# Performance work log

Measured on AMD Instinct MI355X. Metric: run time of the kernel, lower is better.

## Reference

```python
import jax, jax.numpy as jnp
import numpy as np

T_BINS = 1000  # max_time_bins
N_HEADS = 8
BIN = 64


def _ln(x, g, b):
    m = x.mean(-1, keepdims=True)
    v = ((x - m) ** 2).mean(-1, keepdims=True)
    return (x - m) / jnp.sqrt(v + 1e-5) * g + b


def _time_attn(h, td, mask, wq, bq, wk, bk, wv, bv, wo, bo, temb):
    # h: [B,S,D], td: [B,S] float, mask: [B,S] bool
    B, S, D = h.shape
    dk = D // N_HEADS
    q = (h @ wq + bq).reshape(B, S, N_HEADS, dk)
    k = (h @ wk + bk).reshape(B, S, N_HEADS, dk)
    v = (h @ wv + bv).reshape(B, S, N_HEADS, dk)
    scores = jnp.einsum('bqhd,bkhd->bhqk', q, k) / jnp.sqrt(jnp.float32(dk))
    tb = jnp.clip(td.astype(jnp.int32), 0, T_BINS - 1)
    bias = temb[tb].transpose(0, 2, 1)[:, :, None, :]  # [B,H,1,S], key-position bias
    scores = jnp.where(mask[:, None, None, :], scores + bias, -1e9)
    attn = jax.nn.softmax(scores, axis=-1)
    ctx = jnp.einsum('bhqk,bkhd->bqhd', attn, v).reshape(B, S, D)
    return ctx @ wo + bo


def _forward(x, time_deltas,
             emb_event, emb_rel, emb_abs,
             iq_w, iq_b, ik_w, ik_b, iv_w, iv_b, io_w, io_b, i_temb, i_g, i_bt,
             eq_w, eq_b, ek_w, ek_b, ev_w, ev_b, eo_w, eo_b, e_temb, e_g, e_bt,
             w1, b1, w2, b2):
    B, S = x.shape
    NB = S // BIN  # S chosen as a multiple of bin_size -> no padding
    mask = x != 0  # padding_idx = 0
    ee = emb_event.at[0].set(0.0)  # padding_idx row is zero
    rel_bins = jnp.clip(time_deltas.astype(jnp.int32), 0, T_BINS - 1)
    abs_t = jnp.cumsum(jnp.clip(time_deltas, 0.0, None), axis=1)
    abs_bins = jnp.clip(abs_t.astype(jnp.int32), 0, T_BINS - 1)
    h = ee[x] + emb_rel[rel_bins] + emb_abs[abs_bins]  # [B,S,D]
    D = h.shape[-1]
    # intra-bin attention over [B*NB, BIN]
    hi = h.reshape(B * NB, BIN, D)
    ti = time_deltas.reshape(B * NB, BIN)
    mi = mask.reshape(B * NB, BIN)
    hi = _ln(_time_attn(hi, ti, mi, iq_w, iq_b, ik_w, ik_b, iv_w, iv_b, io_w, io_b, i_temb), i_g, i_bt)
    hi = hi.reshape(B, NB, BIN, D)
    # mean pool per bin over valid tokens
    mb = mask.reshape(B, NB, BIN)
    w = mb[..., None].astype(h.dtype)
    denom = jnp.maximum(w.sum(2), 1.0)
    bin_repr = (hi * w).sum(2) / denom  # [B,NB,D]
    bin_mask = mb.any(2)
    abs_masked = jnp.where(mb, abs_t.reshape(B, NB, BIN), 0.0)
    bin_abs = abs_masked.max(2)
    bin_rel = jnp.concatenate(
        [jnp.zeros((B, 1), h.dtype), jnp.maximum(bin_abs[:, 1:] - bin_abs[:, :-1], 0.0)], axis=1)
    h_inter = _ln(_time_attn(bin_repr, bin_rel, bin_mask,
                             eq_w, eq_b, ek_w, ek_b, ev_w, ev_b, eo_w, eo_b, e_temb), e_g, e_bt)
    last_idx = jnp.clip(bin_mask.sum(1) - 1, 0, None)
    last = h_inter[jnp.arange(B), last_idx]  # [B,D]
    return jax.nn.sigmoid(jax.nn.relu(last @ w1 + b1) @ w2 + b2)  # [B,1]


def setup_inputs() -> dict:
    key = jax.random.key(0)
    ks = jax.random.split(key, 24)
    B, S, D, V = 8, 4096, 512, 20000
    sc = 1.0 / np.sqrt(D)
    f32 = jnp.float32
    inp = {
        'x': jax.random.randint(ks[0], (B, S), 0, V),
        'time_deltas': jax.random.uniform(ks[1], (B, S), f32) * 10.0,
        'emb_event': jax.random.normal(ks[2], (V, D), f32) * 0.02,
        'emb_rel': jax.random.normal(ks[3], (T_BINS, D), f32) * 0.02,
        'emb_abs': jax.random.normal(ks[4], (T_BINS, D), f32) * 0.02,
    }
    names = ['iq', 'ik', 'iv', 'io', 'eq', 'ek', 'ev', 'eo']
    for i, n in enumerate(names):
        inp[n + '_w'] = jax.random.normal(ks[5 + i], (D, D), f32) * sc
        inp[n + '_b'] = jnp.zeros((D,), f32)
    inp['i_temb'] = jax.random.normal(ks[13], (T_BINS, N_HEADS), f32) * 0.02
    inp['e_temb'] = jax.random.normal(ks[14], (T_BINS, N_HEADS), f32) * 0.02
    inp['i_g'] = jnp.ones((D,), f32); inp['i_bt'] = jnp.zeros((D,), f32)
    inp['e_g'] = jnp.ones((D,), f32); inp['e_bt'] = jnp.zeros((D,), f32)
    inp['w1'] = jax.random.normal(ks[15], (D, D // 2), f32) * sc
    inp['b1'] = jnp.zeros((D // 2,), f32)
    inp['w2'] = jax.random.normal(ks[16], (D // 2, 1), f32) * np.sqrt(2.0 / D)
    inp['b2'] = jnp.zeros((1,), f32)
    return inp


def reference(x, time_deltas, emb_event, emb_rel, emb_abs,
              iq_w, iq_b, ik_w, ik_b, iv_w, iv_b, io_w, io_b, i_temb, i_g, i_bt,
              eq_w, eq_b, ek_w, ek_b, ev_w, ev_b, eo_w, eo_b, e_temb, e_g, e_bt,
              w1, b1, w2, b2):
    return _forward(x, time_deltas, emb_event, emb_rel, emb_abs,
                    iq_w, iq_b, ik_w, ik_b, iv_w, iv_b, io_w, io_b, i_temb, i_g, i_bt,
                    eq_w, eq_b, ek_w, ek_b, ev_w, ev_b, eo_w, eo_b, e_temb, e_g, e_bt,
                    w1, b1, w2, b2)
```

## Files before the change

kernel.cpp:

```cpp
#include <hip/hip_runtime.h>


typedef __attribute__((ext_vector_type(8))) short bf16x8;
typedef __attribute__((ext_vector_type(4))) float f32x4;

#define DEVI __device__ __forceinline__

DEVI unsigned short f2bf(float f) {
  union { float f; unsigned u; } v; v.f = f;
  unsigned r = v.u + 0x7FFFu + ((v.u >> 16) & 1u);
  return (unsigned short)(r >> 16);
}
DEVI float bf2f(unsigned short u) {
  union { unsigned u; float f; } v; v.u = ((unsigned)u) << 16; return v.f;
}

#define GLOAD_LDS16(gp, lp) \
  __builtin_amdgcn_global_load_lds((const __attribute__((address_space(1))) void*)(gp), \
                                   (__attribute__((address_space(3))) void*)(lp), 16, 0, 0)

struct TPackArgs { const float* s[8]; unsigned short* d[8];
                   const float* bs[6]; float* bd[2]; };

__global__ __launch_bounds__(256) void k_tpack8(TPackArgs args) {
  __shared__ float tile[64][65];
  if (blockIdx.x == 512) {
    int t = threadIdx.x;
    for (int i = t; i < 1536; i += 256) {
      int sel = i >> 9, r = i & 511;
      args.bd[0][i] = args.bs[sel][r];
      args.bd[1][i] = args.bs[3 + sel][r];
    }
    return;
  }
  int mat = blockIdx.x >> 6;
  int tl = blockIdx.x & 63;
  const float* W = args.s[mat];
  unsigned short* Wt = args.d[mat];
  int n0 = (tl & 7) << 6, k0 = (tl >> 3) << 6;
  int t = threadIdx.x, j = t & 63, i0 = t >> 6;
#pragma unroll
  for (int rr = 0; rr < 16; ++rr) {
    int i = rr * 4 + i0;
    tile[i][j] = W[(size_t)(k0 + i) * 512 + n0 + j];
  }
  __syncthreads();
#pragma unroll
  for (int rr = 0; rr < 16; ++rr) {
    int i = rr * 4 + i0;
    Wt[(size_t)(n0 + i) * 512 + k0 + j] = f2bf(tile[j][i]);
  }
}

__global__ __launch_bounds__(64) void k_time(const float* __restrict__ td, const int* __restrict__ x,
    float* __restrict__ abs_t, float* __restrict__ bin_rel, int* __restrict__ bin_mask,
    int* __restrict__ last_idx) {
  int b = blockIdx.x, lane = threadIdx.x;
  const float* row = td + (size_t)b * 4096 + lane * 64;
  const int*   xr  = x  + (size_t)b * 4096 + lane * 64;
  float* out = abs_t + (size_t)b * 4096 + lane * 64;
  float s = 0.f;
  for (int i = 0; i < 64; ++i) s += fmaxf(row[i], 0.f);
  float pre = s;
#pragma unroll
  for (int off = 1; off < 64; off <<= 1) {
    float n = __shfl_up(pre, off, 64);
    if (lane >= off) pre += n;
  }
  float a = pre - s;
  float am = 0.f; int anyv = 0;
  for (int i = 0; i < 64; ++i) {
    a += fmaxf(row[i], 0.f);
    out[i] = a;
    if (xr[i] != 0) { am = fmaxf(am, a); anyv = 1; }
  }
  float prev = __shfl_up(am, 1, 64);
  bin_rel[b * 64 + lane] = (lane == 0) ? 0.f : fmaxf(am - prev, 0.f);
  bin_mask[b * 64 + lane] = anyv;
  unsigned long long bal = __ballot(anyv != 0);
  if (lane == 0) last_idx[b] = max(__popcll(bal) - 1, 0);
}

__global__ __launch_bounds__(256) void k_embed(const int* __restrict__ x, const float* __restrict__ td,
    const float* __restrict__ abs_t, const float* __restrict__ ee, const float* __restrict__ er,
    const float* __restrict__ ea, unsigned short* __restrict__ h) {
  int t = threadIdx.x;
  int tok = blockIdx.x * 4 + (t >> 6);
  int lane = t & 63;
  int c0 = lane * 8;
  int xi = x[tok];
  int rb = (int)td[tok]; rb = min(max(rb, 0), 999);
  int ab = (int)abs_t[tok]; ab = min(max(ab, 0), 999);
  const f32x4* pr = (const f32x4*)(er + (size_t)rb * 512 + c0);
  const f32x4* pa = (const f32x4*)(ea + (size_t)ab * 512 + c0);
  f32x4 s0 = pr[0] + pa[0];
  f32x4 s1 = pr[1] + pa[1];
  if (xi != 0) {
    const f32x4* pe = (const f32x4*)(ee + (size_t)xi * 512 + c0);
    s0 += pe[0]; s1 += pe[1];
  }
  bf16x8 o;
#pragma unroll
  for (int i = 0; i < 4; ++i) { o[i] = (short)f2bf(s0[i]); o[4 + i] = (short)f2bf(s1[i]); }
  *(bf16x8*)(h + (size_t)tok * 512 + c0) = o;
}

DEVI bf16x8 lds_frag32(const unsigned short* buf, int r, int g) {
  int sr = r >> 1;
  int slot = (((r & 1) << 2) | g) ^ (sr & 7);
  return *(const bf16x8*)&buf[sr * 64 + slot * 8];
}

__global__ __launch_bounds__(512, 2) void k_gemm256(const unsigned short* __restrict__ A,
    const unsigned short* __restrict__ Wt, const float* __restrict__ bias,
    unsigned short* __restrict__ Cout, int N, int tiles_n) {
  __shared__ unsigned short lds[4][2][256 * 32];
  int bid = blockIdx.x;
  { int q = (int)gridDim.x >> 3; bid = (bid & 7) * q + (bid >> 3); }
  int by = bid / tiles_n, bx = bid % tiles_n;
  int m0 = by << 8, n0 = bx << 8;
  int t = threadIdx.x;
  int lane = t & 63, w = t >> 6;
  int wm = w >> 2, wn = w & 3;
  int l15 = lane & 15, l4 = lane >> 4;

  auto stageA = [&](int kt) {
    int k0 = kt << 5;
    unsigned short* dst = &lds[kt & 3][0][0];
#pragma unroll
    for (int l = 0; l < 2; ++l) {
      int pos = l * 512 + t;
      int sr = pos >> 3, slot = pos & 7;
      int gp = slot ^ (sr & 7);
      int row = sr * 2 + (gp >> 2);
      GLOAD_LDS16(&A[(size_t)(m0 + row) * 512 + k0 + (gp & 3) * 8], dst + pos * 8);
    }
  };
  auto stageB = [&](int kt) {
    int k0 = kt << 5;
    unsigned short* dst = &lds[kt & 3][1][0];
#pragma unroll
    for (int l = 0; l < 2; ++l) {
      int pos = l * 512 + t;
      int sr = pos >> 3, slot = pos & 7;
      int gp = slot ^ (sr & 7);
      int row = sr * 2 + (gp >> 2);
      GLOAD_LDS16(&Wt[(size_t)(n0 + row) * 512 + k0 + (gp & 3) * 8], dst + pos * 8);
    }
  };

  f32x4 acc[8][4] = {};
  stageA(0); stageB(0);
  stageA(1); stageB(1);
  stageA(2); stageB(2);

  for (int kt = 0; kt < 16; ++kt) {
    if (kt < 14)       asm volatile("s_waitcnt vmcnt(8)" ::: "memory");
    else if (kt == 14) asm volatile("s_waitcnt vmcnt(4)" ::: "memory");
    else               asm volatile("s_waitcnt vmcnt(0)" ::: "memory");
    __builtin_amdgcn_s_barrier();
    const unsigned short* As = &lds[kt & 3][0][0];
    const unsigned short* Bs = &lds[kt & 3][1][0];

    bf16x8 af[4], bb[4];
#pragma unroll
    for (int i = 0; i < 4; ++i) af[i] = lds_frag32(As, wm * 128 + i * 16 + l15, l4);
#pragma unroll
    for (int j = 0; j < 4; ++j) bb[j] = lds_frag32(Bs, wn * 64 + j * 16 + l15, l4);
    if (kt < 13) stageA(kt + 3);
    __builtin_amdgcn_sched_barrier(0);
    __builtin_amdgcn_s_barrier();
    asm volatile("s_waitcnt lgkmcnt(0)" ::: "memory");
    __builtin_amdgcn_sched_barrier(0);
    __builtin_amdgcn_s_setprio(1);
#pragma unroll
    for (int i = 0; i < 4; ++i)
#pragma unroll
      for (int j = 0; j < 4; ++j)
        acc[i][j] = __builtin_amdgcn_mfma_f32_16x16x32_bf16(af[i], bb[j], acc[i][j], 0, 0, 0);
    __builtin_amdgcn_s_setprio(0);

    bf16x8 ah[4];
#pragma unroll
    for (int i = 0; i < 4; ++i) ah[i] = lds_frag32(As, wm * 128 + 64 + i * 16 + l15, l4);
    if (kt < 13) stageB(kt + 3);
    __builtin_amdgcn_sched_barrier(0);
    __builtin_amdgcn_s_barrier();
    asm volatile("s_waitcnt lgkmcnt(0)" ::: "memory");
    __builtin_amdgcn_sched_barrier(0);
    __builtin_amdgcn_s_setprio(1);
#pragma unroll
    for (int i = 0; i < 4; ++i)
#pragma unroll
      for (int j = 0; j < 4; ++j)
        acc[4 + i][j] = __builtin_amdgcn_mfma_f32_16x16x32_bf16(ah[i], bb[j], acc[4 + i][j], 0, 0, 0);
    __builtin_amdgcn_s_setprio(0);
  }
#pragma unroll
  for (int i = 0; i < 8; ++i) {
    int rowb = m0 + wm * 128 + i * 16 + (l4 << 2);
#pragma unroll
    for (int j = 0; j < 4; ++j) {
      int col = n0 + wn * 64 + j * 16 + l15;
      float bv = bias[col];
#pragma unroll
      for (int r = 0; r < 4; ++r)
        Cout[(size_t)(rowb + r) * N + col] = f2bf(acc[i][j][r] + bv);
    }
  }
}

__global__ __launch_bounds__(256) void k_gemm(const unsigned short* __restrict__ A,
    const unsigned short* __restrict__ Wt, const float* __restrict__ bias,
    unsigned short* __restrict__ Cout, int N, int tiles_n) {
  __shared__ unsigned short As[128 * 72];
  __shared__ unsigned short Bs[128 * 72];
  int bx = blockIdx.x % tiles_n;
  int by = blockIdx.x / tiles_n;
  int m0 = by << 7, n0 = bx << 7;
  int t = threadIdx.x;
  int lane = t & 63, w = t >> 6;
  int wm = w >> 1, wn = w & 1;
  f32x4 acc[4][4] = {};
  for (int k0 = 0; k0 < 512; k0 += 64) {
    __syncthreads();
#pragma unroll
    for (int i = 0; i < 4; ++i) {
      int idx = t + i * 256;
      int row = idx >> 3, seg = idx & 7;
      *(bf16x8*)&As[row * 72 + seg * 8] = *(const bf16x8*)&A[(size_t)(m0 + row) * 512 + k0 + seg * 8];
      *(bf16x8*)&Bs[row * 72 + seg * 8] = *(const bf16x8*)&Wt[(size_t)(n0 + row) * 512 + k0 + seg * 8];
    }
    __syncthreads();
#pragma unroll
    for (int ks = 0; ks < 2; ++ks) {
      bf16x8 af[4], bb[4];
#pragma unroll
      for (int i = 0; i < 4; ++i) {
        af[i] = *(const bf16x8*)&As[(wm * 64 + i * 16 + (lane & 15)) * 72 + ks * 32 + (lane >> 4) * 8];
        bb[i] = *(const bf16x8*)&Bs[(wn * 64 + i * 16 + (lane & 15)) * 72 + ks * 32 + (lane >> 4) * 8];
      }
#pragma unroll
      for (int i = 0; i < 4; ++i)
#pragma unroll
        for (int j = 0; j < 4; ++j)
          acc[i][j] = __builtin_amdgcn_mfma_f32_16x16x32_bf16(af[i], bb[j], acc[i][j], 0, 0, 0);
    }
  }
#pragma unroll
  for (int i = 0; i < 4; ++i) {
    int rowb = m0 + wm * 64 + i * 16 + ((lane >> 4) << 2);
#pragma unroll
    for (int j = 0; j < 4; ++j) {
      int col = n0 + wn * 64 + j * 16 + (lane & 15);
      float bv = bias[col];
#pragma unroll
      for (int r = 0; r < 4; ++r)
        Cout[(size_t)(rowb + r) * N + col] = f2bf(acc[i][j][r] + bv);
    }
  }
}

__global__ __launch_bounds__(256) void k_attn(const unsigned short* __restrict__ qkv,
    const float* __restrict__ td, const int* __restrict__ validv,
    const float* __restrict__ temb, unsigned short* __restrict__ ctx) {
  __shared__ float bias_s[4][64];
  __shared__ int valid_s[64];
  __shared__ unsigned short P_s[4][64][72];
  __shared__ unsigned short Vt_s[4][64][72];
  int blk = blockIdx.x >> 1, hg = blockIdx.x & 1;
  int t = threadIdx.x, hl = t >> 6, lane = t & 63;
  int h = hg * 4 + hl;
  size_t base = (size_t)blk * 64;
  if (t < 64) {
    valid_s[t] = (validv[base + t] != 0) ? 1 : 0;
    int tb = (int)td[base + t];
    tb = min(max(tb, 0), 999);
#pragma unroll
    for (int hh = 0; hh < 4; ++hh) bias_s[hh][t] = temb[tb * 8 + hg * 4 + hh];
  }
  {
    const unsigned short* vp = qkv + (base + lane) * 1536 + 1024 + h * 64;
#pragma unroll
    for (int f8 = 0; f8 < 8; ++f8) {
      bf16x8 v8 = *(const bf16x8*)(vp + f8 * 8);
#pragma unroll
      for (int j = 0; j < 8; ++j) Vt_s[hl][f8 * 8 + j][lane] = (unsigned short)v8[j];
    }
  }
  __syncthreads();
  bf16x8 qa[2][4], kb[2][4];
#pragma unroll
  for (int ks = 0; ks < 2; ++ks)
#pragma unroll
    for (int i = 0; i < 4; ++i) {
      int row = i * 16 + (lane & 15);
      int kk = ks * 32 + (lane >> 4) * 8;
      qa[ks][i] = *(const bf16x8*)&qkv[(base + row) * 1536 + h * 64 + kk];
      kb[ks][i] = *(const bf16x8*)&qkv[(base + row) * 1536 + 512 + h * 64 + kk];
    }
  f32x4 acc[4][4] = {};
#pragma unroll
  for (int ks = 0; ks < 2; ++ks)
#pragma unroll
    for (int i = 0; i < 4; ++i)
#pragma unroll
      for (int j = 0; j < 4; ++j)
        acc[i][j] = __builtin_amdgcn_mfma_f32_16x16x32_bf16(qa[ks][i], kb[ks][j], acc[i][j], 0, 0, 0);
#pragma unroll
  for (int i = 0; i < 4; ++i) {
#pragma unroll
    for (int r = 0; r < 4; ++r) {
      float sv[4];
#pragma unroll
      for (int j = 0; j < 4; ++j) {
        int key = j * 16 + (lane & 15);
        float s = acc[i][j][r] * 0.125f;
        sv[j] = valid_s[key] ? (s + bias_s[hl][key]) : -1e9f;
      }
      float m = fmaxf(fmaxf(sv[0], sv[1]), fmaxf(sv[2], sv[3]));
#pragma unroll
      for (int off = 1; off < 16; off <<= 1) m = fmaxf(m, __shfl_xor(m, off, 64));
      float p[4], sum = 0.f;
#pragma unroll
      for (int j = 0; j < 4; ++j) { p[j] = __expf(sv[j] - m); sum += p[j]; }
#pragma unroll
      for (int off = 1; off < 16; off <<= 1) sum += __shfl_xor(sum, off, 64);
      float inv = 1.f / sum;
      int row = i * 16 + ((lane >> 4) << 2) + r;
#pragma unroll
      for (int j = 0; j < 4; ++j) P_s[hl][row][j * 16 + (lane & 15)] = f2bf(p[j] * inv);
    }
  }
  __syncthreads();
  f32x4 acc2[4][4] = {};
#pragma unroll
  for (int ks = 0; ks < 2; ++ks) {
    bf16x8 pa[4], vb[4];
    int kk = ks * 32 + (lane >> 4) * 8;
#pragma unroll
    for (int i = 0; i < 4; ++i) {
      pa[i] = *(const bf16x8*)&P_s[hl][i * 16 + (lane & 15)][kk];
      vb[i] = *(const bf16x8*)&Vt_s[hl][i * 16 + (lane & 15)][kk];
    }
#pragma unroll
    for (int i = 0; i < 4; ++i)
#pragma unroll
      for (int j = 0; j < 4; ++j)
        acc2[i][j] = __builtin_amdgcn_mfma_f32_16x16x32_bf16(pa[i], vb[j], acc2[i][j], 0, 0, 0);
  }
#pragma unroll
  for (int i = 0; i < 4; ++i) {
    int rowb = i * 16 + ((lane >> 4) << 2);
#pragma unroll
    for (int j = 0; j < 4; ++j) {
      int col = h * 64 + j * 16 + (lane & 15);
#pragma unroll
      for (int r = 0; r < 4; ++r)
        ctx[(base + rowb + r) * 512 + col] = f2bf(acc2[i][j][r]);
    }
  }
}

__global__ __launch_bounds__(256) void k_lnpool(const unsigned short* __restrict__ X,
    const float* __restrict__ g, const float* __restrict__ bt,
    const int* __restrict__ validv, unsigned short* __restrict__ out) {
  __shared__ float pool_s[4][512];
  __shared__ int cnt_s[4];
  int blk = blockIdx.x;
  int t = threadIdx.x, w = t >> 6, lane = t & 63;
  float gv[8], bv[8];
#pragma unroll
  for (int i = 0; i < 8; ++i) { gv[i] = g[lane * 8 + i]; bv[i] = bt[lane * 8 + i]; }
  float psum[8] = {0.f, 0.f, 0.f, 0.f, 0.f, 0.f, 0.f, 0.f};
  int cnt = 0;
  for (int r0 = 0; r0 < 16; ++r0) {
    int row = blk * 64 + w * 16 + r0;
    bf16x8 xv = *(const bf16x8*)(X + (size_t)row * 512 + lane * 8);
    float xa[8];
#pragma unroll
    for (int i = 0; i < 8; ++i) xa[i] = bf2f((unsigned short)xv[i]);
    float s = 0.f;
#pragma unroll
    for (int i = 0; i < 8; ++i) s += xa[i];
#pragma unroll
    for (int off = 1; off < 64; off <<= 1) s += __shfl_xor(s, off, 64);
    float mean = s * (1.f / 512.f);
    float vsum = 0.f;
#pragma unroll
    for (int i = 0; i < 8; ++i) { float d = xa[i] - mean; vsum += d * d; }
#pragma unroll
    for (int off = 1; off < 64; off <<= 1) vsum += __shfl_xor(vsum, off, 64);
    float rstd = rsqrtf(vsum * (1.f / 512.f) + 1e-5f);
    if (validv[row] != 0) {
      cnt++;
#pragma unroll
      for (int i = 0; i < 8; ++i) psum[i] += (xa[i] - mean) * rstd * gv[i] + bv[i];
    }
  }
#pragma unroll
  for (int i = 0; i < 8; ++i) pool_s[w][lane * 8 + i] = psum[i];
  if (lane == 0) cnt_s[w] = cnt;
  __syncthreads();
  int total = cnt_s[0] + cnt_s[1] + cnt_s[2] + cnt_s[3];
  float denom = fmaxf((float)total, 1.f);
  for (int c = t; c < 512; c += 256) {
    float v = (pool_s[0][c] + pool_s[1][c] + pool_s[2][c] + pool_s[3][c]) / denom;
    out[(size_t)blk * 512 + c] = f2bf(v);
  }
}

__global__ __launch_bounds__(256) void k_final(const unsigned short* __restrict__ proj2,
    const int* __restrict__ last_idx, const float* __restrict__ g, const float* __restrict__ bt,
    const float* __restrict__ w1, const float* __restrict__ b1,
    const float* __restrict__ w2, const float* __restrict__ b2, float* __restrict__ outp) {
  __shared__ float row_s[512];
  __shared__ float red_s[4];
  __shared__ float red2_s[4];
  int b = blockIdx.x, t = threadIdx.x;
  const unsigned short* rp = proj2 + (size_t)(b * 64 + last_idx[b]) * 512;
  float v0 = bf2f(rp[t]), v1 = bf2f(rp[t + 256]);
  float s = v0 + v1;
#pragma unroll
  for (int off = 1; off < 64; off <<= 1) s += __shfl_xor(s, off, 64);
  if ((t & 63) == 0) red_s[t >> 6] = s;
  __syncthreads();
  float mean = (red_s[0] + red_s[1] + red_s[2] + red_s[3]) * (1.f / 512.f);
  float d0 = v0 - mean, d1 = v1 - mean;
  float vs = d0 * d0 + d1 * d1;
#pragma unroll
  for (int off = 1; off < 64; off <<= 1) vs += __shfl_xor(vs, off, 64);
  if ((t & 63) == 0) red2_s[t >> 6] = vs;
  __syncthreads();
  float rstd = rsqrtf((red2_s[0] + red2_s[1] + red2_s[2] + red2_s[3]) * (1.f / 512.f) + 1e-5f);
  row_s[t]       = d0 * rstd * g[t]       + bt[t];
  row_s[t + 256] = d1 * rstd * g[t + 256] + bt[t + 256];
  __syncthreads();
  float acc = b1[t];
  for (int k = 0; k < 512; ++k) acc += row_s[k] * w1[(size_t)k * 256 + t];
  float hv = fmaxf(acc, 0.f) * w2[t];
#pragma unroll
  for (int off = 1; off < 64; off <<= 1) hv += __shfl_xor(hv, off, 64);
  if ((t & 63) == 0) red_s[t >> 6] = hv;
  __syncthreads();
  if (t == 0) {
    float o = red_s[0] + red_s[1] + red_s[2] + red_s[3] + b2[0];
    outp[b] = 1.f / (1.f + __expf(-o));
  }
}

extern "C" void kernel_launch(void* const* d_in, const int* in_sizes, int n_in,
                              void* d_out, int out_size, void* d_ws, size_t ws_size,
                              hipStream_t stream) {
  const int*   x    = (const int*)d_in[0];
  const float* td   = (const float*)d_in[1];
  const float* ee   = (const float*)d_in[2];
  const float* er   = (const float*)d_in[3];
  const float* ea   = (const float*)d_in[4];
  const float* iq_w = (const float*)d_in[5];  const float* iq_b = (const float*)d_in[6];
  const float* ik_w = (const float*)d_in[7];  const float* ik_b = (const float*)d_in[8];
  const float* iv_w = (const float*)d_in[9];  const float* iv_b = (const float*)d_in[10];
  const float* io_w = (const float*)d_in[11]; const float* io_b = (const float*)d_in[12];
  const float* eq_w = (const float*)d_in[13]; const float* eq_b = (const float*)d_in[14];
  const float* ek_w = (const float*)d_in[15]; const float* ek_b = (const float*)d_in[16];
  const float* ev_w = (const float*)d_in[17]; const float* ev_b = (const float*)d_in[18];
  const float* eo_w = (const float*)d_in[19]; const float* eo_b = (const float*)d_in[20];
  const float* i_temb = (const float*)d_in[21];
  const float* e_temb = (const float*)d_in[22];
  const float* i_g  = (const float*)d_in[23]; const float* i_bt = (const float*)d_in[24];
  const float* e_g  = (const float*)d_in[25]; const float* e_bt = (const float*)d_in[26];
  const float* w1   = (const float*)d_in[27]; const float* b1   = (const float*)d_in[28];
  const float* w2   = (const float*)d_in[29]; const float* b2   = (const float*)d_in[30];

  char* ws = (char*)d_ws;
  size_t off = 0;
  auto alloc = [&](size_t nb) { size_t r = off; off += (nb + 255) & ~(size_t)255; return r; };
  float* abs_t    = (float*)(ws + alloc((size_t)32768 * 4));
  float* bin_rel  = (float*)(ws + alloc(512 * 4));
  int*   bin_mask = (int*)(ws + alloc(512 * 4));
  int*   last_idx = (int*)(ws + alloc(64));
  unsigned short* wqkv_i = (unsigned short*)(ws + alloc((size_t)1536 * 512 * 2));
  unsigned short* wo_i   = (unsigned short*)(ws + alloc((size_t)512 * 512 * 2));
  unsigned short* wqkv_e = (unsigned short*)(ws + alloc((size_t)1536 * 512 * 2));
  unsigned short* wo_e   = (unsigned short*)(ws + alloc((size_t)512 * 512 * 2));
  float* bqkv_i = (float*)(ws + alloc(1536 * 4));
  float* bqkv_e = (float*)(ws + alloc(1536 * 4));
  unsigned short* hbuf = (unsigned short*)(ws + alloc((size_t)32768 * 512 * 2));
  char* big = ws + alloc((size_t)32768 * 1536 * 2);
  unsigned short* qkvbuf = (unsigned short*)big;
  unsigned short* projbuf = (unsigned short*)big;
  unsigned short* bin_repr = (unsigned short*)(ws + alloc((size_t)512 * 512 * 2));
  char* small = ws + alloc((size_t)512 * 1536 * 2);
  unsigned short* qkv2 = (unsigned short*)small;
  unsigned short* proj2 = (unsigned short*)small;
  unsigned short* ctx2 = (unsigned short*)(ws + alloc((size_t)512 * 512 * 2));

  TPackArgs tp;
  tp.s[0] = iq_w; tp.d[0] = wqkv_i;
  tp.s[1] = ik_w; tp.d[1] = wqkv_i + (size_t)512 * 512;
  tp.s[2] = iv_w; tp.d[2] = wqkv_i + (size_t)1024 * 512;
  tp.s[3] = io_w; tp.d[3] = wo_i;
  tp.s[4] = eq_w; tp.d[4] = wqkv_e;
  tp.s[5] = ek_w; tp.d[5] = wqkv_e + (size_t)512 * 512;
  tp.s[6] = ev_w; tp.d[6] = wqkv_e + (size_t)1024 * 512;
  tp.s[7] = eo_w; tp.d[7] = wo_e;
  tp.bs[0] = iq_b; tp.bs[1] = ik_b; tp.bs[2] = iv_b;
  tp.bs[3] = eq_b; tp.bs[4] = ek_b; tp.bs[5] = ev_b;
  tp.bd[0] = bqkv_i; tp.bd[1] = bqkv_e;
  k_tpack8<<<513, 256, 0, stream>>>(tp);

  k_time<<<8, 64, 0, stream>>>(td, x, abs_t, bin_rel, bin_mask, last_idx);

  k_embed<<<8192, 256, 0, stream>>>(x, td, abs_t, ee, er, ea, hbuf);

  k_gemm256<<<128 * 6, 512, 0, stream>>>(hbuf, wqkv_i, bqkv_i, qkvbuf, 1536, 6);
  k_attn<<<1024, 256, 0, stream>>>(qkvbuf, td, x, i_temb, hbuf);
  k_gemm256<<<128 * 2, 512, 0, stream>>>(hbuf, wo_i, io_b, projbuf, 512, 2);
  k_lnpool<<<512, 256, 0, stream>>>(projbuf, i_g, i_bt, x, bin_repr);

  k_gemm<<<4 * 12, 256, 0, stream>>>(bin_repr, wqkv_e, bqkv_e, qkv2, 1536, 12);
  k_attn<<<16, 256, 0, stream>>>(qkv2, bin_rel, bin_mask, e_temb, ctx2);
  k_gemm<<<4 * 4, 256, 0, stream>>>(ctx2, wo_e, eo_b, proj2, 512, 4);

  k_final<<<8, 256, 0, stream>>>(proj2, last_idx, e_g, e_bt, w1, b1, w2, b2, (float*)d_out);
}
```

Measured before the change: 234.2 us.

## Fuse intra-bin output projection with LayerNorm and mean pooling

Result: no change. 231.1 us (-1.3%).

```diff
diff --git a/kernel.cpp b/kernel.cpp
--- a/kernel.cpp
+++ b/kernel.cpp
@@ -85,24 +85,27 @@
     const float* __restrict__ abs_t, const float* __restrict__ ee, const float* __restrict__ er,
     const float* __restrict__ ea, unsigned short* __restrict__ h) {
   int t = threadIdx.x;
-  int tok = blockIdx.x * 4 + (t >> 6);
   int lane = t & 63;
   int c0 = lane * 8;
-  int xi = x[tok];
-  int rb = (int)td[tok]; rb = min(max(rb, 0), 999);
-  int ab = (int)abs_t[tok]; ab = min(max(ab, 0), 999);
-  const f32x4* pr = (const f32x4*)(er + (size_t)rb * 512 + c0);
-  const f32x4* pa = (const f32x4*)(ea + (size_t)ab * 512 + c0);
-  f32x4 s0 = pr[0] + pa[0];
-  f32x4 s1 = pr[1] + pa[1];
-  if (xi != 0) {
-    const f32x4* pe = (const f32x4*)(ee + (size_t)xi * 512 + c0);
-    s0 += pe[0]; s1 += pe[1];
-  }
-  bf16x8 o;
-#pragma unroll
-  for (int i = 0; i < 4; ++i) { o[i] = (short)f2bf(s0[i]); o[4 + i] = (short)f2bf(s1[i]); }
-  *(bf16x8*)(h + (size_t)tok * 512 + c0) = o;
+#pragma unroll
+  for (int it = 0; it < 4; ++it) {
+    int tok = blockIdx.x * 16 + it * 4 + (t >> 6);
+    int xi = x[tok];
+    int rb = (int)td[tok]; rb = min(max(rb, 0), 999);
+    int ab = (int)abs_t[tok]; ab = min(max(ab, 0), 999);
+    const f32x4* pr = (const f32x4*)(er + (size_t)rb * 512 + c0);
+    const f32x4* pa = (const f32x4*)(ea + (size_t)ab * 512 + c0);
+    f32x4 s0 = pr[0] + pa[0];
+    f32x4 s1 = pr[1] + pa[1];
+    if (xi != 0) {
+      const f32x4* pe = (const f32x4*)(ee + (size_t)xi * 512 + c0);
+      s0 += pe[0]; s1 += pe[1];
+    }
+    bf16x8 o;
+#pragma unroll
+    for (int i = 0; i < 4; ++i) { o[i] = (short)f2bf(s0[i]); o[4 + i] = (short)f2bf(s1[i]); }
+    *(bf16x8*)(h + (size_t)tok * 512 + c0) = o;
+  }
 }
 
 DEVI bf16x8 lds_frag32(const unsigned short* buf, int r, int g) {
@@ -168,7 +171,6 @@
 #pragma unroll
     for (int j = 0; j < 4; ++j) bb[j] = lds_frag32(Bs, wn * 64 + j * 16 + l15, l4);
     if (kt < 13) stageA(kt + 3);
-    __builtin_amdgcn_sched_barrier(0);
     __builtin_amdgcn_s_barrier();
     asm volatile("s_waitcnt lgkmcnt(0)" ::: "memory");
     __builtin_amdgcn_sched_barrier(0);
@@ -184,7 +186,6 @@
 #pragma unroll
     for (int i = 0; i < 4; ++i) ah[i] = lds_frag32(As, wm * 128 + 64 + i * 16 + l15, l4);
     if (kt < 13) stageB(kt + 3);
-    __builtin_amdgcn_sched_barrier(0);
     __builtin_amdgcn_s_barrier();
     asm volatile("s_waitcnt lgkmcnt(0)" ::: "memory");
     __builtin_amdgcn_sched_barrier(0);
@@ -206,6 +207,174 @@
 #pragma unroll
       for (int r = 0; r < 4; ++r)
         Cout[(size_t)(rowb + r) * N + col] = f2bf(acc[i][j][r] + bv);
+    }
+  }
+}
+
+__global__ __launch_bounds__(512, 2) void k_oproj(const unsigned short* __restrict__ ctx,
+    const unsigned short* __restrict__ WoT, const float* __restrict__ bo,
+    const int* __restrict__ x, const float* __restrict__ g, const float* __restrict__ bt,
+    unsigned short* __restrict__ bin_repr) {
+  __shared__ unsigned short ldsA[4][128 * 32];
+  __shared__ unsigned short ldsB[2][512 * 32];
+  int bid = blockIdx.x;
+  { int q = (int)gridDim.x >> 3; bid = (bid & 7) * q + (bid >> 3); }
+  int m0 = bid << 7;
+  int t = threadIdx.x;
+  int lane = t & 63, w = t >> 6;
+  int l15 = lane & 15, l4 = lane >> 4;
+
+  auto stageA = [&](int kt) {
+    int k0 = kt << 5;
+    unsigned short* dst = &ldsA[kt & 3][0];
+    int pos = t;
+    int sr = pos >> 3, slot = pos & 7;
+    int gp = slot ^ (sr & 7);
+    int row = sr * 2 + (gp >> 2);
+    GLOAD_LDS16(&ctx[(size_t)(m0 + row) * 512 + k0 + (gp & 3) * 8], dst + pos * 8);
+  };
+  auto stageB = [&](int kt) {
+    int k0 = kt << 5;
+    unsigned short* dst = &ldsB[kt & 1][0];
+#pragma unroll
+    for (int l = 0; l < 4; ++l) {
+      int pos = l * 512 + t;
+      int sr = pos >> 3, slot = pos & 7;
+      int gp = slot ^ (sr & 7);
+      int row = sr * 2 + (gp >> 2);
+      GLOAD_LDS16(&WoT[(size_t)row * 512 + k0 + (gp & 3) * 8], dst + pos * 8);
+    }
+  };
+
+  f32x4 acc[8][4] = {};
+  stageB(0); stageA(0); stageA(1); stageA(2); stageB(1);
+
+  for (int kt = 0; kt < 16; ++kt) {
+    if (kt == 0)      asm volatile("s_waitcnt vmcnt(6)" ::: "memory");
+    else if (kt < 14) asm volatile("s_waitcnt vmcnt(1)" ::: "memory");
+    else              asm volatile("s_waitcnt vmcnt(0)" ::: "memory");
+    __builtin_amdgcn_s_barrier();
+    const unsigned short* As = &ldsA[kt & 3][0];
+    const unsigned short* Bs = &ldsB[kt & 1][0];
+
+    bf16x8 af[4], bb[4];
+#pragma unroll
+    for (int i = 0; i < 4; ++i) af[i] = lds_frag32(As, i * 16 + l15, l4);
+#pragma unroll
+    for (int j = 0; j < 4; ++j) bb[j] = lds_frag32(Bs, w * 64 + j * 16 + l15, l4);
+    if (kt >= 1 && kt <= 14) stageB(kt + 1);
+    __builtin_amdgcn_s_barrier();
+    asm volatile("s_waitcnt lgkmcnt(0)" ::: "memory");
+    __builtin_amdgcn_sched_barrier(0);
+    __builtin_amdgcn_s_setprio(1);
+#pragma unroll
+    for (int i = 0; i < 4; ++i)
+#pragma unroll
+      for (int j = 0; j < 4; ++j)
+        acc[i][j] = __builtin_amdgcn_mfma_f32_16x16x32_bf16(af[i], bb[j], acc[i][j], 0, 0, 0);
+    __builtin_amdgcn_s_setprio(0);
+
+    bf16x8 ah[4];
+#pragma unroll
+    for (int i = 0; i < 4; ++i) ah[i] = lds_frag32(As, 64 + i * 16 + l15, l4);
+    if (kt <= 12) stageA(kt + 3);
+    __builtin_amdgcn_s_barrier();
+    asm volatile("s_waitcnt lgkmcnt(0)" ::: "memory");
+    __builtin_amdgcn_sched_barrier(0);
+    __builtin_amdgcn_s_setprio(1);
+#pragma unroll
+    for (int i = 0; i < 4; ++i)
+#pragma unroll
+      for (int j = 0; j < 4; ++j)
+        acc[4 + i][j] = __builtin_amdgcn_mfma_f32_16x16x32_bf16(ah[i], bb[j], acc[4 + i][j], 0, 0, 0);
+    __builtin_amdgcn_s_setprio(0);
+  }
+
+  __syncthreads();
+  float* red   = (float*)&ldsA[0][0];
+  float* meanL = red + 128 * 9;
+  float* rstdL = meanL + 128;
+  int*   valL  = (int*)(rstdL + 128);
+  int*   cntL  = valL + 128;
+
+  int cols[4]; float bov[4], gv[4], bv[4];
+#pragma unroll
+  for (int j = 0; j < 4; ++j) {
+    cols[j] = w * 64 + j * 16 + l15;
+    bov[j] = bo[cols[j]]; gv[j] = g[cols[j]]; bv[j] = bt[cols[j]];
+  }
+  if (t < 128) {
+    int v = (x[m0 + t] != 0) ? 1 : 0;
+    valL[t] = v;
+    unsigned long long bal = __ballot(v != 0);
+    if ((t & 63) == 0) cntL[t >> 6] = __popcll(bal);
+  }
+#pragma unroll
+  for (int i = 0; i < 8; ++i)
+#pragma unroll
+    for (int r = 0; r < 4; ++r) {
+      float s = (acc[i][0][r] + bov[0]) + (acc[i][1][r] + bov[1]) +
+                (acc[i][2][r] + bov[2]) + (acc[i][3][r] + bov[3]);
+#pragma unroll
+      for (int off = 1; off < 16; off <<= 1) s += __shfl_xor(s, off, 64);
+      if (l15 == 0) red[(i * 16 + l4 * 4 + r) * 9 + w] = s;
+    }
+  __syncthreads();
+  if (t < 128) {
+    float m = 0.f;
+#pragma unroll
+    for (int ww = 0; ww < 8; ++ww) m += red[t * 9 + ww];
+    meanL[t] = m * (1.f / 512.f);
+  }
+  __syncthreads();
+#pragma unroll
+  for (int i = 0; i < 8; ++i)
+#pragma unroll
+    for (int r = 0; r < 4; ++r) {
+      float m = meanL[i * 16 + l4 * 4 + r];
+      float s = 0.f;
+#pragma unroll
+      for (int j = 0; j < 4; ++j) { float d = acc[i][j][r] + bov[j] - m; s += d * d; }
+#pragma unroll
+      for (int off = 1; off < 16; off <<= 1) s += __shfl_xor(s, off, 64);
+      if (l15 == 0) red[(i * 16 + l4 * 4 + r) * 9 + w] = s;
+    }
+  __syncthreads();
+  if (t < 128) {
+    float vsum = 0.f;
+#pragma unroll
+    for (int ww = 0; ww < 8; ++ww) vsum += red[t * 9 + ww];
+    rstdL[t] = rsqrtf(vsum * (1.f / 512.f) + 1e-5f);
+  }
+  __syncthreads();
+  float p0[4] = {0.f, 0.f, 0.f, 0.f}, p1[4] = {0.f, 0.f, 0.f, 0.f};
+#pragma unroll
+  for (int i = 0; i < 8; ++i)
+#pragma unroll
+    for (int r = 0; r < 4; ++r) {
+      int row = i * 16 + l4 * 4 + r;
+      if (valL[row]) {
+        float m = meanL[row], rs = rstdL[row];
+#pragma unroll
+        for (int j = 0; j < 4; ++j) {
+          float y = (acc[i][j][r] + bov[j] - m) * rs * gv[j] + bv[j];
+          if (i < 4) p0[j] += y; else p1[j] += y;
+        }
+      }
+    }
+#pragma unroll
+  for (int j = 0; j < 4; ++j) {
+    p0[j] += __shfl_xor(p0[j], 16, 64); p0[j] += __shfl_xor(p0[j], 32, 64);
+    p1[j] += __shfl_xor(p1[j], 16, 64); p1[j] += __shfl_xor(p1[j], 32, 64);
+  }
+  float d0 = 1.f / fmaxf((float)cntL[0], 1.f);
+  float d1 = 1.f / fmaxf((float)cntL[1], 1.f);
+  if (l4 == 0) {
+    int binr = (m0 >> 6);
+#pragma unroll
+    for (int j = 0; j < 4; ++j) {
+      bin_repr[(size_t)binr * 512 + cols[j]]       = f2bf(p0[j] * d0);
+      bin_repr[(size_t)(binr + 1) * 512 + cols[j]] = f2bf(p1[j] * d1);
     }
   }
 }
@@ -359,54 +528,6 @@
       for (int r = 0; r < 4; ++r)
         ctx[(base + rowb + r) * 512 + col] = f2bf(acc2[i][j][r]);
     }
-  }
-}
-
-__global__ __launch_bounds__(256) void k_lnpool(const unsigned short* __restrict__ X,
-    const float* __restrict__ g, const float* __restrict__ bt,
-    const int* __restrict__ validv, unsigned short* __restrict__ out) {
-  __shared__ float pool_s[4][512];
-  __shared__ int cnt_s[4];
-  int blk = blockIdx.x;
-  int t = threadIdx.x, w = t >> 6, lane = t & 63;
-  float gv[8], bv[8];
-#pragma unroll
-  for (int i = 0; i < 8; ++i) { gv[i] = g[lane * 8 + i]; bv[i] = bt[lane * 8 + i]; }
-  float psum[8] = {0.f, 0.f, 0.f, 0.f, 0.f, 0.f, 0.f, 0.f};
-  int cnt = 0;
-  for (int r0 = 0; r0 < 16; ++r0) {
-    int row = blk * 64 + w * 16 + r0;
-    bf16x8 xv = *(const bf16x8*)(X + (size_t)row * 512 + lane * 8);
-    float xa[8];
-#pragma unroll
-    for (int i = 0; i < 8; ++i) xa[i] = bf2f((unsigned short)xv[i]);
-    float s = 0.f;
-#pragma unroll
-    for (int i = 0; i < 8; ++i) s += xa[i];
-#pragma unroll
-    for (int off = 1; off < 64; off <<= 1) s += __shfl_xor(s, off, 64);
-    float mean = s * (1.f / 512.f);
-    float vsum = 0.f;
-#pragma unroll
-    for (int i = 0; i < 8; ++i) { float d = xa[i] - mean; vsum += d * d; }
-#pragma unroll
-    for (int off = 1; off < 64; off <<= 1) vsum += __shfl_xor(vsum, off, 64);
-    float rstd = rsqrtf(vsum * (1.f / 512.f) + 1e-5f);
-    if (validv[row] != 0) {
-      cnt++;
-#pragma unroll
-      for (int i = 0; i < 8; ++i) psum[i] += (xa[i] - mean) * rstd * gv[i] + bv[i];
-    }
-  }
-#pragma unroll
-  for (int i = 0; i < 8; ++i) pool_s[w][lane * 8 + i] = psum[i];
-  if (lane == 0) cnt_s[w] = cnt;
-  __syncthreads();
-  int total = cnt_s[0] + cnt_s[1] + cnt_s[2] + cnt_s[3];
-  float denom = fmaxf((float)total, 1.f);
-  for (int c = t; c < 512; c += 256) {
-    float v = (pool_s[0][c] + pool_s[1][c] + pool_s[2][c] + pool_s[3][c]) / denom;
-    out[(size_t)blk * 512 + c] = f2bf(v);
   }
 }
 
@@ -486,9 +607,7 @@
   float* bqkv_i = (float*)(ws + alloc(1536 * 4));
   float* bqkv_e = (float*)(ws + alloc(1536 * 4));
   unsigned short* hbuf = (unsigned short*)(ws + alloc((size_t)32768 * 512 * 2));
-  char* big = ws + alloc((size_t)32768 * 1536 * 2);
-  unsigned short* qkvbuf = (unsigned short*)big;
-  unsigned short* projbuf = (unsigned short*)big;
+  unsigned short* qkvbuf = (unsigned short*)(ws + alloc((size_t)32768 * 1536 * 2));
   unsigned short* bin_repr = (unsigned short*)(ws + alloc((size_t)512 * 512 * 2));
   char* small = ws + alloc((size_t)512 * 1536 * 2);
   unsigned short* qkv2 = (unsigned short*)small;
@@ -511,12 +630,11 @@
 
   k_time<<<8, 64, 0, stream>>>(td, x, abs_t, bin_rel, bin_mask, last_idx);
 
-  k_embed<<<8192, 256, 0, stream>>>(x, td, abs_t, ee, er, ea, hbuf);
+  k_embed<<<2048, 256, 0, stream>>>(x, td, abs_t, ee, er, ea, hbuf);
 
   k_gemm256<<<128 * 6, 512, 0, stream>>>(hbuf, wqkv_i, bqkv_i, qkvbuf, 1536, 6);
   k_attn<<<1024, 256, 0, stream>>>(qkvbuf, td, x, i_temb, hbuf);
-  k_gemm256<<<128 * 2, 512, 0, stream>>>(hbuf, wo_i, io_b, projbuf, 512, 2);
-  k_lnpool<<<512, 256, 0, stream>>>(projbuf, i_g, i_bt, x, bin_repr);
+  k_oproj<<<256, 512, 0, stream>>>(hbuf, wo_i, io_b, x, i_g, i_bt, bin_repr);
 
   k_gemm<<<4 * 12, 256, 0, stream>>>(bin_repr, wqkv_e, bqkv_e, qkv2, 1536, 12);
   k_attn<<<16, 256, 0, stream>>>(qkv2, bin_rel, bin_mask, e_temb, ctx2);
```
